# Kernel optimization log

Measured on AMD Instinct MI355X. Metric: run time of the kernel, lower is better.

## Reference

```python
import jax, jax.numpy as jnp
import numpy as np

N_NODES = 16384
N_EDGES = 524288
N_GRAPHS = 256
IN_CH = 128
H_CH = 128   # per-head channels
HEADS = 2
LAYER_DIM = HEADS * H_CH  # 256, concat=True
POOL_DIM = 3 * LAYER_DIM  # 768
OUT_CH = 1
NEG_SLOPE = 0.2


def setup_inputs() -> dict:
    key = jax.random.key(0)
    ks = jax.random.split(key, 20)
    s = lambda k, shape, fan: jax.random.normal(k, shape, jnp.float32) * (1.0 / np.sqrt(fan))
    inp = {
        "x": jax.random.normal(ks[0], (N_NODES, IN_CH), jnp.float32),
        "edge_index": jax.random.randint(ks[1], (2, N_EDGES), 0, N_NODES, jnp.int64),
        "batch": jnp.sort(jax.random.randint(ks[2], (N_NODES,), 0, N_GRAPHS, jnp.int64)),
        # GATv2 layer 1 (in=128)
        "Wl1": s(ks[3], (IN_CH, LAYER_DIM), IN_CH), "Wr1": s(ks[4], (IN_CH, LAYER_DIM), IN_CH),
        "att1": s(ks[5], (HEADS, H_CH), H_CH), "b1": jnp.zeros((LAYER_DIM,), jnp.float32),
        # GATv2 layer 2 (in=256)
        "Wl2": s(ks[6], (LAYER_DIM, LAYER_DIM), LAYER_DIM), "Wr2": s(ks[7], (LAYER_DIM, LAYER_DIM), LAYER_DIM),
        "att2": s(ks[8], (HEADS, H_CH), H_CH), "b2": jnp.zeros((LAYER_DIM,), jnp.float32),
        # GATv2 layer 3 (in=256)
        "Wl3": s(ks[9], (LAYER_DIM, LAYER_DIM), LAYER_DIM), "Wr3": s(ks[10], (LAYER_DIM, LAYER_DIM), LAYER_DIM),
        "att3": s(ks[11], (HEADS, H_CH), H_CH), "b3": jnp.zeros((LAYER_DIM,), jnp.float32),
        # FFN (dropout inactive at eval)
        "fW1": s(ks[12], (POOL_DIM, POOL_DIM), POOL_DIM), "fb1": jnp.zeros((POOL_DIM,), jnp.float32),
        "fW2": s(ks[13], (POOL_DIM, OUT_CH), POOL_DIM), "fb2": jnp.zeros((OUT_CH,), jnp.float32),
    }
    return inp


def _gatv2(x, src, dst, Wl, Wr, att, b):
    """PyG GATv2Conv: per-edge score a . LeakyReLU(Wl x_src + Wr x_dst),
    softmax over incoming edges per destination, weighted scatter-add of Wl x_src."""
    n = x.shape[0]
    xl = (x @ Wl).reshape(n, HEADS, H_CH)  # source messages
    xr = (x @ Wr).reshape(n, HEADS, H_CH)  # target query
    e = jax.nn.leaky_relu(xl[src] + xr[dst], NEG_SLOPE)          # [E,H,C]
    logits = jnp.einsum('ehc,hc->eh', e, att)                    # [E,H]
    m = jax.ops.segment_max(logits, dst, num_segments=n)         # per-dst max (self-loops guarantee nonempty)
    ev = jnp.exp(logits - m[dst])
    denom = jax.ops.segment_sum(ev, dst, num_segments=n)
    alpha = ev / denom[dst]                                       # [E,H]
    out = jax.ops.segment_sum(alpha[..., None] * xl[src], dst, num_segments=n)  # [N,H,C]
    return out.reshape(n, LAYER_DIM) + b


def reference(x, edge_index, batch, Wl1, Wr1, att1, b1, Wl2, Wr2, att2, b2,
              Wl3, Wr3, att3, b3, fW1, fb1, fW2, fb2):
    n = x.shape[0]
    loops = jnp.arange(n, dtype=edge_index.dtype)
    src = jnp.concatenate([edge_index[0], loops])  # add_self_loops=True default
    dst = jnp.concatenate([edge_index[1], loops])
    h1 = _gatv2(x, src, dst, Wl1, Wr1, att1, b1)
    h2 = _gatv2(h1, src, dst, Wl2, Wr2, att2, b2)
    h3 = _gatv2(h2, src, dst, Wl3, Wr3, att3, b3)
    pool = lambda h: jax.ops.segment_sum(h, batch, num_segments=N_GRAPHS)
    h = jnp.concatenate([pool(h1), pool(h2), pool(h3)], axis=1)   # [G,768]
    h = jax.nn.relu(h @ fW1 + fb1)
    return h @ fW2 + fb2                                           # [G,1]
```

## Files before the change

kernel.cpp:

```cpp
#include <hip/hip_runtime.h>

#define NNODES 16384
#define NEDGES 524288
#define NETOT  (NEDGES + NNODES)
#define NGRAPH 256

typedef __attribute__((ext_vector_type(8))) short short8;
typedef __attribute__((ext_vector_type(4))) float f32x4;
typedef __attribute__((ext_vector_type(2))) float f32x2;

__device__ __forceinline__ float b2f(unsigned short u){
  union { unsigned int i; float f; } v; v.i = ((unsigned int)u) << 16; return v.f;
}
__device__ __forceinline__ unsigned short f2b(float f){
  union { float f; unsigned int i; } v; v.f = f;
  unsigned int r = v.i + 0x7FFFu + ((v.i >> 16) & 1u);
  return (unsigned short)(r >> 16);
}
__device__ __forceinline__ f32x2 unpack2(unsigned int u){
  union { unsigned int i; float f; } lo, hi;
  lo.i = u << 16; hi.i = u & 0xFFFF0000u;
  f32x2 r; r[0] = lo.f; r[1] = hi.f; return r;
}

__global__ void __launch_bounds__(256) zero_deg(int* __restrict__ deg){
  deg[blockIdx.x * 256 + threadIdx.x] = 0;
}

__global__ void __launch_bounds__(256) count_deg(const int* __restrict__ ei, int* __restrict__ deg){
  int i = blockIdx.x * 256 + threadIdx.x;
  int d = (i < NEDGES) ? ei[NEDGES + i] : (i - NEDGES);
  atomicAdd(&deg[d], 1);
}

__global__ void __launch_bounds__(256) scan1(const int* __restrict__ deg,
                                             int* __restrict__ incl, int* __restrict__ bsum){
  __shared__ int ws[4];
  const int b = blockIdx.x, t = threadIdx.x, lane = t & 63, w = t >> 6;
  int v = deg[b * 256 + t];
  int x = v;
  #pragma unroll
  for(int o = 1; o < 64; o <<= 1){ int u = __shfl_up(x, o, 64); if(lane >= o) x += u; }
  if(lane == 63) ws[w] = x;
  __syncthreads();
  int add = 0;
  #pragma unroll
  for(int j = 0; j < 4; j++) if(j < w) add += ws[j];
  incl[b * 256 + t] = x + add;
  if(t == 255) bsum[b] = x + add;
}

__global__ void __launch_bounds__(64) scan2(const int* __restrict__ bsum, int* __restrict__ boff){
  const int t = threadIdx.x;
  int v = bsum[t];
  int x = v;
  #pragma unroll
  for(int o = 1; o < 64; o <<= 1){ int u = __shfl_up(x, o, 64); if(t >= o) x += u; }
  boff[t] = x - v;
}

__global__ void __launch_bounds__(256) scan3(const int* __restrict__ deg, const int* __restrict__ incl,
                                             const int* __restrict__ boff,
                                             int* __restrict__ row_off, int* __restrict__ cursor){
  const int b = blockIdx.x, t = threadIdx.x;
  const int i = b * 256 + t;
  int inc = incl[i] + boff[b];
  row_off[i + 1] = inc;
  cursor[i] = inc - deg[i];
  if(i == 0) row_off[0] = 0;
}

__global__ void __launch_bounds__(256) fill_csr(const int* __restrict__ ei, int* __restrict__ cursor,
                                                int* __restrict__ col_src){
  int i = blockIdx.x * 256 + threadIdx.x;
  int s, d;
  if(i < NEDGES){ s = ei[i]; d = ei[NEDGES + i]; }
  else          { s = i - NEDGES; d = s; }
  int p = atomicAdd(&cursor[d], 1);
  col_src[p] = s;
}

__global__ void __launch_bounds__(256) convX(const float* __restrict__ x, unsigned short* __restrict__ xb){
  int i = blockIdx.x * 256 + threadIdx.x;
  xb[i] = f2b(x[i]);
}

template<int K>
__global__ void __launch_bounds__(256) convW(const float* __restrict__ Wl, const float* __restrict__ Wr,
                                             unsigned short* __restrict__ Wt){
  int i = blockIdx.x * 256 + threadIdx.x;
  int k = i >> 9, c = i & 511;
  float val = (c < 256) ? Wl[(size_t)k * 256 + c] : Wr[(size_t)k * 256 + (c - 256)];
  Wt[(size_t)c * K + k] = f2b(val);
}

template<int K>
__global__ void __launch_bounds__(256) gemm_xw(const unsigned short* __restrict__ A,
                                               const unsigned short* __restrict__ Wt,
                                               unsigned short* __restrict__ Cout){
  __shared__ unsigned short As[128][40];
  __shared__ unsigned short Bs[128][40];
  const int t = threadIdx.x;
  const int rowbase = blockIdx.x * 128;
  const int colbase = blockIdx.y * 128;
  const int wave = t >> 6, lane = t & 63;
  const int lrow = lane & 15, kg = lane >> 4;

  f32x4 acc[2][8] = {};

  for(int kt = 0; kt < K; kt += 32){
    {
      int oct = t & 3, r = t >> 2;
      const unsigned short* ga = A + (size_t)(rowbase + r) * K + kt + oct * 8;
      short8 v0 = *(const short8*)ga;
      short8 v1 = *(const short8*)(ga + 64 * K);
      *(short8*)(&As[r][oct * 8])      = v0;
      *(short8*)(&As[r + 64][oct * 8]) = v1;
    }
    {
      int n = t & 127, kh = (t >> 7) * 16;
      const unsigned short* gw = Wt + (size_t)(colbase + n) * K + kt + kh;
      short8 v0 = *(const short8*)gw;
      short8 v1 = *(const short8*)(gw + 8);
      *(short8*)(&Bs[n][kh])     = v0;
      *(short8*)(&Bs[n][kh + 8]) = v1;
    }
    __syncthreads();
    short8 afrag[2], bfrag[8];
    afrag[0] = *(const short8*)(&As[wave * 32 + lrow][kg * 8]);
    afrag[1] = *(const short8*)(&As[wave * 32 + 16 + lrow][kg * 8]);
    #pragma unroll
    for(int fc = 0; fc < 8; fc++) bfrag[fc] = *(const short8*)(&Bs[fc * 16 + lrow][kg * 8]);
    #pragma unroll
    for(int rf = 0; rf < 2; rf++)
      #pragma unroll
      for(int fc = 0; fc < 8; fc++)
        acc[rf][fc] = __builtin_amdgcn_mfma_f32_16x16x32_bf16(afrag[rf], bfrag[fc], acc[rf][fc], 0, 0, 0);
    __syncthreads();
  }
  #pragma unroll
  for(int rf = 0; rf < 2; rf++)
    #pragma unroll
    for(int fc = 0; fc < 8; fc++)
      #pragma unroll
      for(int r = 0; r < 4; r++){
        int row = rowbase + wave * 32 + rf * 16 + kg * 4 + r;
        int col = colbase + fc * 16 + lrow;
        Cout[(size_t)row * 512 + col] = f2b(acc[rf][fc][r]);
      }
}

__global__ void __launch_bounds__(256) edge_agg(const unsigned short* __restrict__ xlb,
                                                const int* __restrict__ row_off,
                                                const int* __restrict__ col_src,
                                                const float* __restrict__ att,
                                                const float* __restrict__ bias,
                                                unsigned short* __restrict__ hout){
  const int n = (blockIdx.x * 256 + threadIdx.x) >> 6;
  const int lane = threadIdx.x & 63;
  const int eg = lane >> 5;
  const int c0 = (lane & 31) * 8;
  f32x2 xr0, xr1, xr2, xr3, at0, at1, at2, at3;
  {
    uint4 v = *(const uint4*)(xlb + (size_t)n * 512 + 256 + c0);
    xr0 = unpack2(v.x); xr1 = unpack2(v.y); xr2 = unpack2(v.z); xr3 = unpack2(v.w);
    at0 = *(const f32x2*)(att + c0);
    at1 = *(const f32x2*)(att + c0 + 2);
    at2 = *(const f32x2*)(att + c0 + 4);
    at3 = *(const f32x2*)(att + c0 + 6);
  }
  float s = 0.f;
  f32x2 ac0 = {0.f, 0.f}, ac1 = {0.f, 0.f}, ac2 = {0.f, 0.f}, ac3 = {0.f, 0.f};
  const int beg = row_off[n], end = row_off[n + 1];
  for(int ch = beg; ch < end; ch += 64){
    int idx = ch + lane;
    int si = (idx < end) ? col_src[idx] : 0;
    int cnt = end - ch; if(cnt > 64) cnt = 64;
    for(int k = 0; k < cnt; k += 2){
      int kk = k + eg;
      int src = __shfl(si, kk);
      uint4 v = *(const uint4*)(xlb + (size_t)src * 512 + c0);
      f32x2 x0 = unpack2(v.x), x1 = unpack2(v.y), x2 = unpack2(v.z), x3 = unpack2(v.w);
      f32x2 e0 = x0 + xr0, e1 = x1 + xr1, e2 = x2 + xr2, e3 = x3 + xr3;
      e0 = __builtin_elementwise_max(e0, e0 * 0.2f);
      e1 = __builtin_elementwise_max(e1, e1 * 0.2f);
      e2 = __builtin_elementwise_max(e2, e2 * 0.2f);
      e3 = __builtin_elementwise_max(e3, e3 * 0.2f);
      f32x2 p2 = e0 * at0;
      p2 += e1 * at1;
      p2 += e2 * at2;
      p2 += e3 * at3;
      float p = p2[0] + p2[1];
      p += __shfl_xor(p, 1); p += __shfl_xor(p, 2);
      p += __shfl_xor(p, 4); p += __shfl_xor(p, 8);
      float pe = (kk < cnt) ? __expf(p) : 0.f;
      s += pe;
      f32x2 pe2 = {pe, pe};
      ac0 += pe2 * x0; ac1 += pe2 * x1; ac2 += pe2 * x2; ac3 += pe2 * x3;
    }
  }
  s += __shfl_xor(s, 32);
  #pragma unroll
  for(int i = 0; i < 2; i++){
    ac0[i] += __shfl_xor(ac0[i], 32); ac1[i] += __shfl_xor(ac1[i], 32);
    ac2[i] += __shfl_xor(ac2[i], 32); ac3[i] += __shfl_xor(ac3[i], 32);
  }
  if(eg == 0){
    float inv = 1.f / s;
    ushort4 o0, o1;
    o0.x = f2b(fmaf(ac0[0], inv, bias[c0 + 0]));
    o0.y = f2b(fmaf(ac0[1], inv, bias[c0 + 1]));
    o0.z = f2b(fmaf(ac1[0], inv, bias[c0 + 2]));
    o0.w = f2b(fmaf(ac1[1], inv, bias[c0 + 3]));
    o1.x = f2b(fmaf(ac2[0], inv, bias[c0 + 4]));
    o1.y = f2b(fmaf(ac2[1], inv, bias[c0 + 5]));
    o1.z = f2b(fmaf(ac3[0], inv, bias[c0 + 6]));
    o1.w = f2b(fmaf(ac3[1], inv, bias[c0 + 7]));
    *(ushort4*)(hout + (size_t)n * 256 + c0)     = o0;
    *(ushort4*)(hout + (size_t)n * 256 + c0 + 4) = o1;
  }
}

__device__ __forceinline__ int lbound(const int* __restrict__ a, int n, int v){
  int lo = 0, hi = n;
  while(lo < hi){ int mid = (lo + hi) >> 1; if(a[mid] < v) lo = mid + 1; else hi = mid; }
  return lo;
}

__global__ void __launch_bounds__(256) pool_accum(const unsigned short* __restrict__ h,
                                                  const int* __restrict__ batch,
                                                  float* __restrict__ pool, int slot){
  __shared__ float red[8][264];
  const int g = blockIdx.x, t = threadIdx.x;
  const int ng = t >> 5, c0 = (t & 31) * 8;
  const int lo = lbound(batch, NNODES, g);
  const int hi = lbound(batch, NNODES, g + 1);
  f32x2 a0 = {0.f,0.f}, a1 = {0.f,0.f}, a2 = {0.f,0.f}, a3 = {0.f,0.f};
  for(int node = lo + ng; node < hi; node += 8){
    uint4 v = *(const uint4*)(h + (size_t)node * 256 + c0);
    a0 += unpack2(v.x); a1 += unpack2(v.y); a2 += unpack2(v.z); a3 += unpack2(v.w);
  }
  red[ng][c0 + 0] = a0[0]; red[ng][c0 + 1] = a0[1];
  red[ng][c0 + 2] = a1[0]; red[ng][c0 + 3] = a1[1];
  red[ng][c0 + 4] = a2[0]; red[ng][c0 + 5] = a2[1];
  red[ng][c0 + 6] = a3[0]; red[ng][c0 + 7] = a3[1];
  __syncthreads();
  float s = 0.f;
  #pragma unroll
  for(int i = 0; i < 8; i++) s += red[i][t];
  pool[(size_t)g * 768 + slot * 256 + t] = s;
}

__global__ void __launch_bounds__(256) ffn1(const float* __restrict__ pool,
                                            const float* __restrict__ fW1,
                                            const float* __restrict__ fb1,
                                            float* __restrict__ hidden){
  __shared__ float ap[32][65];
  __shared__ float ws[64][33];
  const int t = threadIdx.x;
  const int cb = blockIdx.x * 32;
  const int gb = blockIdx.y * 32;
  const int tc = t & 31, tg = t >> 5;
  float acc[4] = {};
  for(int kc = 0; kc < 768; kc += 64){
    {
      int g_l = t >> 3, j8 = (t & 7) * 8;
      const float* gp = pool + (size_t)(gb + g_l) * 768 + kc + j8;
      #pragma unroll
      for(int i = 0; i < 8; i++) ap[g_l][j8 + i] = gp[i];
    }
    {
      int c_l = t & 31, k0 = (t >> 5) * 8;
      #pragma unroll
      for(int i = 0; i < 8; i++) ws[k0 + i][c_l] = fW1[(size_t)(kc + k0 + i) * 768 + cb + c_l];
    }
    __syncthreads();
    #pragma unroll
    for(int k = 0; k < 64; k++){
      float w = ws[k][tc];
      #pragma unroll
      for(int i = 0; i < 4; i++) acc[i] = fmaf(ap[tg * 4 + i][k], w, acc[i]);
    }
    __syncthreads();
  }
  float b = fb1[cb + tc];
  #pragma unroll
  for(int i = 0; i < 4; i++)
    hidden[(size_t)(gb + tg * 4 + i) * 768 + cb + tc] = fmaxf(acc[i] + b, 0.f);
}

__global__ void __launch_bounds__(256) ffn2(const float* __restrict__ hidden,
                                            const float* __restrict__ fW2,
                                            const float* __restrict__ fb2,
                                            float* __restrict__ out){
  const int g = (blockIdx.x * 256 + threadIdx.x) >> 6;
  const int lane = threadIdx.x & 63;
  float p = 0.f;
  for(int i = lane; i < 768; i += 64) p += hidden[(size_t)g * 768 + i] * fW2[i];
  #pragma unroll
  for(int o = 32; o > 0; o >>= 1) p += __shfl_xor(p, o, 64);
  if(lane == 0) out[g] = p + fb2[0];
}

extern "C" void kernel_launch(void* const* d_in, const int* in_sizes, int n_in,
                              void* d_out, int out_size, void* d_ws, size_t ws_size,
                              hipStream_t stream){
  const float* x    = (const float*)d_in[0];
  const int* ei     = (const int*)d_in[1];
  const int* batch  = (const int*)d_in[2];
  const float* Wl[3]  = {(const float*)d_in[3],  (const float*)d_in[7],  (const float*)d_in[11]};
  const float* Wr[3]  = {(const float*)d_in[4],  (const float*)d_in[8],  (const float*)d_in[12]};
  const float* att[3] = {(const float*)d_in[5],  (const float*)d_in[9],  (const float*)d_in[13]};
  const float* bp[3]  = {(const float*)d_in[6],  (const float*)d_in[10], (const float*)d_in[14]};
  const float* fW1 = (const float*)d_in[15];
  const float* fb1 = (const float*)d_in[16];
  const float* fW2 = (const float*)d_in[17];
  const float* fb2 = (const float*)d_in[18];

  char* ws = (char*)d_ws;
  size_t off = 0;
  auto alloc = [&](size_t sz){ size_t p = off; off += (sz + 255) & ~(size_t)255; return p; };
  int* deg      = (int*)(ws + alloc((size_t)NNODES * 4));
  int* rowoff   = (int*)(ws + alloc((size_t)(NNODES + 1) * 4));
  int* cursor   = (int*)(ws + alloc((size_t)NNODES * 4));
  int* colsrc   = (int*)(ws + alloc((size_t)NETOT * 4));
  int* incl     = (int*)(ws + alloc((size_t)NNODES * 4));
  int* bsum     = (int*)(ws + alloc(64 * 4));
  int* boff     = (int*)(ws + alloc(64 * 4));
  unsigned short* xb  = (unsigned short*)(ws + alloc((size_t)NNODES * 128 * 2));
  unsigned short* Wt  = (unsigned short*)(ws + alloc((size_t)512 * 256 * 2));
  unsigned short* xlb = (unsigned short*)(ws + alloc((size_t)NNODES * 512 * 2));
  unsigned short* hA  = (unsigned short*)(ws + alloc((size_t)NNODES * 256 * 2));
  unsigned short* hB  = (unsigned short*)(ws + alloc((size_t)NNODES * 256 * 2));
  float* pool   = (float*)(ws + alloc((size_t)NGRAPH * 768 * 4));
  float* hidden = (float*)(ws + alloc((size_t)NGRAPH * 768 * 4));

  zero_deg<<<NNODES / 256, 256, 0, stream>>>(deg);
  count_deg<<<NETOT / 256, 256, 0, stream>>>(ei, deg);
  scan1<<<NNODES / 256, 256, 0, stream>>>(deg, incl, bsum);
  scan2<<<1, 64, 0, stream>>>(bsum, boff);
  scan3<<<NNODES / 256, 256, 0, stream>>>(deg, incl, boff, rowoff, cursor);
  fill_csr<<<NETOT / 256, 256, 0, stream>>>(ei, cursor, colsrc);

  dim3 ggrid(NNODES / 128, 4);

  convX<<<NNODES * 128 / 256, 256, 0, stream>>>(x, xb);
  convW<128><<<128 * 512 / 256, 256, 0, stream>>>(Wl[0], Wr[0], Wt);
  gemm_xw<128><<<ggrid, 256, 0, stream>>>(xb, Wt, xlb);
  edge_agg<<<NNODES / 4, 256, 0, stream>>>(xlb, rowoff, colsrc, att[0], bp[0], hA);
  pool_accum<<<NGRAPH, 256, 0, stream>>>(hA, batch, pool, 0);

  convW<256><<<256 * 512 / 256, 256, 0, stream>>>(Wl[1], Wr[1], Wt);
  gemm_xw<256><<<ggrid, 256, 0, stream>>>(hA, Wt, xlb);
  edge_agg<<<NNODES / 4, 256, 0, stream>>>(xlb, rowoff, colsrc, att[1], bp[1], hB);
  pool_accum<<<NGRAPH, 256, 0, stream>>>(hB, batch, pool, 1);

  convW<256><<<256 * 512 / 256, 256, 0, stream>>>(Wl[2], Wr[2], Wt);
  gemm_xw<256><<<ggrid, 256, 0, stream>>>(hB, Wt, xlb);
  edge_agg<<<NNODES / 4, 256, 0, stream>>>(xlb, rowoff, colsrc, att[2], bp[2], hA);
  pool_accum<<<NGRAPH, 256, 0, stream>>>(hA, batch, pool, 2);

  ffn1<<<dim3(768 / 32, NGRAPH / 32), 256, 0, stream>>>(pool, fW1, fb1, hidden);
  ffn2<<<NGRAPH / 4, 256, 0, stream>>>(hidden, fW2, fb2, (float*)d_out);
}
```

Before: 290.1 us.

## Merge prep kernels, fold scan2 into scan3, widen edge_agg to 16 channels per lane

```diff
diff --git a/kernel.cpp b/kernel.cpp
--- a/kernel.cpp
+++ b/kernel.cpp
@@ -50,21 +50,20 @@
   if(t == 255) bsum[b] = x + add;
 }
 
-__global__ void __launch_bounds__(64) scan2(const int* __restrict__ bsum, int* __restrict__ boff){
-  const int t = threadIdx.x;
-  int v = bsum[t];
-  int x = v;
-  #pragma unroll
-  for(int o = 1; o < 64; o <<= 1){ int u = __shfl_up(x, o, 64); if(t >= o) x += u; }
-  boff[t] = x - v;
-}
-
 __global__ void __launch_bounds__(256) scan3(const int* __restrict__ deg, const int* __restrict__ incl,
-                                             const int* __restrict__ boff,
+                                             const int* __restrict__ bsum,
                                              int* __restrict__ row_off, int* __restrict__ cursor){
+  __shared__ int boff_s;
   const int b = blockIdx.x, t = threadIdx.x;
+  if(t < 64){
+    int v = (t < b) ? bsum[t] : 0;
+    #pragma unroll
+    for(int o = 32; o > 0; o >>= 1) v += __shfl_xor(v, o, 64);
+    if(t == 0) boff_s = v;
+  }
+  __syncthreads();
   const int i = b * 256 + t;
-  int inc = incl[i] + boff[b];
+  int inc = incl[i] + boff_s;
   row_off[i + 1] = inc;
   cursor[i] = inc - deg[i];
   if(i == 0) row_off[0] = 0;
@@ -80,15 +79,24 @@
   col_src[p] = s;
 }
 
-__global__ void __launch_bounds__(256) convX(const float* __restrict__ x, unsigned short* __restrict__ xb){
-  int i = blockIdx.x * 256 + threadIdx.x;
-  xb[i] = f2b(x[i]);
-}
-
-template<int K>
-__global__ void __launch_bounds__(256) convW(const float* __restrict__ Wl, const float* __restrict__ Wr,
-                                             unsigned short* __restrict__ Wt){
-  int i = blockIdx.x * 256 + threadIdx.x;
+__global__ void __launch_bounds__(256) prep(const float* __restrict__ x,
+                                            const float* __restrict__ Wl1, const float* __restrict__ Wr1,
+                                            const float* __restrict__ Wl2, const float* __restrict__ Wr2,
+                                            const float* __restrict__ Wl3, const float* __restrict__ Wr3,
+                                            unsigned short* __restrict__ xb,
+                                            unsigned short* __restrict__ Wt1,
+                                            unsigned short* __restrict__ Wt2,
+                                            unsigned short* __restrict__ Wt3){
+  const int b = blockIdx.x, t = threadIdx.x;
+  if(b < 8192){
+    int i = b * 256 + t;
+    xb[i] = f2b(x[i]);
+    return;
+  }
+  const float *Wl, *Wr; unsigned short* Wt; int K, i;
+  if(b < 8192 + 256){ Wl = Wl1; Wr = Wr1; Wt = Wt1; K = 128; i = (b - 8192) * 256 + t; }
+  else if(b < 8192 + 256 + 512){ Wl = Wl2; Wr = Wr2; Wt = Wt2; K = 256; i = (b - 8448) * 256 + t; }
+  else { Wl = Wl3; Wr = Wr3; Wt = Wt3; K = 256; i = (b - 8960) * 256 + t; }
   int k = i >> 9, c = i & 511;
   float val = (c < 256) ? Wl[(size_t)k * 256 + c] : Wr[(size_t)k * 256 + (c - 256)];
   Wt[(size_t)c * K + k] = f2b(val);
@@ -158,66 +166,68 @@
                                                 unsigned short* __restrict__ hout){
   const int n = (blockIdx.x * 256 + threadIdx.x) >> 6;
   const int lane = threadIdx.x & 63;
-  const int eg = lane >> 5;
-  const int c0 = (lane & 31) * 8;
-  f32x2 xr0, xr1, xr2, xr3, at0, at1, at2, at3;
+  const int eg = lane >> 4;
+  const int c0 = (lane & 15) * 16;
+  f32x2 xr[8], at[8];
   {
-    uint4 v = *(const uint4*)(xlb + (size_t)n * 512 + 256 + c0);
-    xr0 = unpack2(v.x); xr1 = unpack2(v.y); xr2 = unpack2(v.z); xr3 = unpack2(v.w);
-    at0 = *(const f32x2*)(att + c0);
-    at1 = *(const f32x2*)(att + c0 + 2);
-    at2 = *(const f32x2*)(att + c0 + 4);
-    at3 = *(const f32x2*)(att + c0 + 6);
+    const unsigned short* xp = xlb + (size_t)n * 512 + 256 + c0;
+    uint4 v0 = *(const uint4*)xp;
+    uint4 v1 = *(const uint4*)(xp + 8);
+    xr[0] = unpack2(v0.x); xr[1] = unpack2(v0.y); xr[2] = unpack2(v0.z); xr[3] = unpack2(v0.w);
+    xr[4] = unpack2(v1.x); xr[5] = unpack2(v1.y); xr[6] = unpack2(v1.z); xr[7] = unpack2(v1.w);
+    #pragma unroll
+    for(int i = 0; i < 8; i++) at[i] = *(const f32x2*)(att + c0 + 2 * i);
   }
   float s = 0.f;
-  f32x2 ac0 = {0.f, 0.f}, ac1 = {0.f, 0.f}, ac2 = {0.f, 0.f}, ac3 = {0.f, 0.f};
+  f32x2 ac[8] = {};
   const int beg = row_off[n], end = row_off[n + 1];
   for(int ch = beg; ch < end; ch += 64){
     int idx = ch + lane;
     int si = (idx < end) ? col_src[idx] : 0;
     int cnt = end - ch; if(cnt > 64) cnt = 64;
-    for(int k = 0; k < cnt; k += 2){
+    for(int k = 0; k < cnt; k += 4){
       int kk = k + eg;
       int src = __shfl(si, kk);
-      uint4 v = *(const uint4*)(xlb + (size_t)src * 512 + c0);
-      f32x2 x0 = unpack2(v.x), x1 = unpack2(v.y), x2 = unpack2(v.z), x3 = unpack2(v.w);
-      f32x2 e0 = x0 + xr0, e1 = x1 + xr1, e2 = x2 + xr2, e3 = x3 + xr3;
-      e0 = __builtin_elementwise_max(e0, e0 * 0.2f);
-      e1 = __builtin_elementwise_max(e1, e1 * 0.2f);
-      e2 = __builtin_elementwise_max(e2, e2 * 0.2f);
-      e3 = __builtin_elementwise_max(e3, e3 * 0.2f);
-      f32x2 p2 = e0 * at0;
-      p2 += e1 * at1;
-      p2 += e2 * at2;
-      p2 += e3 * at3;
+      const unsigned short* gp = xlb + (size_t)src * 512 + c0;
+      uint4 v0 = *(const uint4*)gp;
+      uint4 v1 = *(const uint4*)(gp + 8);
+      f32x2 x0 = unpack2(v0.x), x1 = unpack2(v0.y), x2 = unpack2(v0.z), x3 = unpack2(v0.w);
+      f32x2 x4 = unpack2(v1.x), x5 = unpack2(v1.y), x6 = unpack2(v1.z), x7 = unpack2(v1.w);
+      f32x2 e, p2;
+      e = x0 + xr[0]; e = __builtin_elementwise_max(e, e * 0.2f); p2  = e * at[0];
+      e = x1 + xr[1]; e = __builtin_elementwise_max(e, e * 0.2f); p2 += e * at[1];
+      e = x2 + xr[2]; e = __builtin_elementwise_max(e, e * 0.2f); p2 += e * at[2];
+      e = x3 + xr[3]; e = __builtin_elementwise_max(e, e * 0.2f); p2 += e * at[3];
+      e = x4 + xr[4]; e = __builtin_elementwise_max(e, e * 0.2f); p2 += e * at[4];
+      e = x5 + xr[5]; e = __builtin_elementwise_max(e, e * 0.2f); p2 += e * at[5];
+      e = x6 + xr[6]; e = __builtin_elementwise_max(e, e * 0.2f); p2 += e * at[6];
+      e = x7 + xr[7]; e = __builtin_elementwise_max(e, e * 0.2f); p2 += e * at[7];
       float p = p2[0] + p2[1];
-      p += __shfl_xor(p, 1); p += __shfl_xor(p, 2);
-      p += __shfl_xor(p, 4); p += __shfl_xor(p, 8);
+      p += __shfl_xor(p, 1); p += __shfl_xor(p, 2); p += __shfl_xor(p, 4);
       float pe = (kk < cnt) ? __expf(p) : 0.f;
       s += pe;
       f32x2 pe2 = {pe, pe};
-      ac0 += pe2 * x0; ac1 += pe2 * x1; ac2 += pe2 * x2; ac3 += pe2 * x3;
-    }
-  }
-  s += __shfl_xor(s, 32);
-  #pragma unroll
-  for(int i = 0; i < 2; i++){
-    ac0[i] += __shfl_xor(ac0[i], 32); ac1[i] += __shfl_xor(ac1[i], 32);
-    ac2[i] += __shfl_xor(ac2[i], 32); ac3[i] += __shfl_xor(ac3[i], 32);
+      ac[0] += pe2 * x0; ac[1] += pe2 * x1; ac[2] += pe2 * x2; ac[3] += pe2 * x3;
+      ac[4] += pe2 * x4; ac[5] += pe2 * x5; ac[6] += pe2 * x6; ac[7] += pe2 * x7;
+    }
+  }
+  s += __shfl_xor(s, 16); s += __shfl_xor(s, 32);
+  #pragma unroll
+  for(int i = 0; i < 8; i++){
+    ac[i][0] += __shfl_xor(ac[i][0], 16); ac[i][0] += __shfl_xor(ac[i][0], 32);
+    ac[i][1] += __shfl_xor(ac[i][1], 16); ac[i][1] += __shfl_xor(ac[i][1], 32);
   }
   if(eg == 0){
     float inv = 1.f / s;
-    ushort4 o0, o1;
-    o0.x = f2b(fmaf(ac0[0], inv, bias[c0 + 0]));
-    o0.y = f2b(fmaf(ac0[1], inv, bias[c0 + 1]));
-    o0.z = f2b(fmaf(ac1[0], inv, bias[c0 + 2]));
-    o0.w = f2b(fmaf(ac1[1], inv, bias[c0 + 3]));
-    o1.x = f2b(fmaf(ac2[0], inv, bias[c0 + 4]));
-    o1.y = f2b(fmaf(ac2[1], inv, bias[c0 + 5]));
-    o1.z = f2b(fmaf(ac3[0], inv, bias[c0 + 6]));
-    o1.w = f2b(fmaf(ac3[1], inv, bias[c0 + 7]));
-    *(ushort4*)(hout + (size_t)n * 256 + c0)     = o0;
-    *(ushort4*)(hout + (size_t)n * 256 + c0 + 4) = o1;
+    unsigned short o[16];
+    #pragma unroll
+    for(int i = 0; i < 8; i++){
+      o[2 * i]     = f2b(fmaf(ac[i][0], inv, bias[c0 + 2 * i]));
+      o[2 * i + 1] = f2b(fmaf(ac[i][1], inv, bias[c0 + 2 * i + 1]));
+    }
+    unsigned short* hp = hout + (size_t)n * 256 + c0;
+    *(uint4*)hp       = *(const uint4*)&o[0];
+    *(uint4*)(hp + 8) = *(const uint4*)&o[8];
   }
 }
 
@@ -326,9 +336,10 @@
   int* colsrc   = (int*)(ws + alloc((size_t)NETOT * 4));
   int* incl     = (int*)(ws + alloc((size_t)NNODES * 4));
   int* bsum     = (int*)(ws + alloc(64 * 4));
-  int* boff     = (int*)(ws + alloc(64 * 4));
   unsigned short* xb  = (unsigned short*)(ws + alloc((size_t)NNODES * 128 * 2));
-  unsigned short* Wt  = (unsigned short*)(ws + alloc((size_t)512 * 256 * 2));
+  unsigned short* Wt1 = (unsigned short*)(ws + alloc((size_t)512 * 128 * 2));
+  unsigned short* Wt2 = (unsigned short*)(ws + alloc((size_t)512 * 256 * 2));
+  unsigned short* Wt3 = (unsigned short*)(ws + alloc((size_t)512 * 256 * 2));
   unsigned short* xlb = (unsigned short*)(ws + alloc((size_t)NNODES * 512 * 2));
   unsigned short* hA  = (unsigned short*)(ws + alloc((size_t)NNODES * 256 * 2));
   unsigned short* hB  = (unsigned short*)(ws + alloc((size_t)NNODES * 256 * 2));
@@ -337,26 +348,23 @@
 
   zero_deg<<<NNODES / 256, 256, 0, stream>>>(deg);
   count_deg<<<NETOT / 256, 256, 0, stream>>>(ei, deg);
+  prep<<<8192 + 256 + 512 + 512, 256, 0, stream>>>(x, Wl[0], Wr[0], Wl[1], Wr[1], Wl[2], Wr[2],
+                                                   xb, Wt1, Wt2, Wt3);
   scan1<<<NNODES / 256, 256, 0, stream>>>(deg, incl, bsum);
-  scan2<<<1, 64, 0, stream>>>(bsum, boff);
-  scan3<<<NNODES / 256, 256, 0, stream>>>(deg, incl, boff, rowoff, cursor);
+  scan3<<<NNODES / 256, 256, 0, stream>>>(deg, incl, bsum, rowoff, cursor);
   fill_csr<<<NETOT / 256, 256, 0, stream>>>(ei, cursor, colsrc);
 
   dim3 ggrid(NNODES / 128, 4);
 
-  convX<<<NNODES * 128 / 256, 256, 0, stream>>>(x, xb);
-  convW<128><<<128 * 512 / 256, 256, 0, stream>>>(Wl[0], Wr[0], Wt);
-  gemm_xw<128><<<ggrid, 256, 0, stream>>>(xb, Wt, xlb);
+  gemm_xw<128><<<ggrid, 256, 0, stream>>>(xb, Wt1, xlb);
   edge_agg<<<NNODES / 4, 256, 0, stream>>>(xlb, rowoff, colsrc, att[0], bp[0], hA);
   pool_accum<<<NGRAPH, 256, 0, stream>>>(hA, batch, pool, 0);
 
-  convW<256><<<256 * 512 / 256, 256, 0, stream>>>(Wl[1], Wr[1], Wt);
-  gemm_xw<256><<<ggrid, 256, 0, stream>>>(hA, Wt, xlb);
+  gemm_xw<256><<<ggrid, 256, 0, stream>>>(hA, Wt2, xlb);
   edge_agg<<<NNODES / 4, 256, 0, stream>>>(xlb, rowoff, colsrc, att[1], bp[1], hB);
   pool_accum<<<NGRAPH, 256, 0, stream>>>(hB, batch, pool, 1);
 
-  convW<256><<<256 * 512 / 256, 256, 0, stream>>>(Wl[2], Wr[2], Wt);
-  gemm_xw<256><<<ggrid, 256, 0, stream>>>(hB, Wt, xlb);
+  gemm_xw<256><<<ggrid, 256, 0, stream>>>(hB, Wt3, xlb);
   edge_agg<<<NNODES / 4, 256, 0, stream>>>(xlb, rowoff, colsrc, att[2], bp[2], hA);
   pool_accum<<<NGRAPH, 256, 0, stream>>>(hA, batch, pool, 2);
 
```

Measured after the change: 286.3 us. No clear change (-1.3%).
